# Kernel tuning notes

Measured on AMD Instinct MI355X. Metric: run time of the kernel, lower is better.

Reference implementation:

```python
import jax, jax.numpy as jnp
import numpy as np
from jax import lax

NQ = 4      # num_qubits
DEPTH = 2
DIM = 2 ** NQ  # 16

def _maxpool2(x):
    # MaxPool2d(kernel_size=2, stride=1), NCHW
    return lax.reduce_window(x, -jnp.inf, lax.max, (1, 1, 2, 2), (1, 1, 1, 1), 'VALID')

def _conv(x, w, b, stride, pad):
    y = lax.conv_general_dilated(x, w, (stride, stride), [(pad, pad), (pad, pad)],
                                 dimension_numbers=('NCHW', 'OIHW', 'NCHW'))
    return y + b[None, :, None, None]

def _apply_1q(state, gate, q):
    # state: (B, 16) complex64; gate: (2,2) shared or (B,2,2) per-sample. wire 0 = MSB.
    B = state.shape[0]
    s = state.reshape(B, 2 ** q, 2, 2 ** (NQ - 1 - q))
    sub = 'ij,bljr->blir' if gate.ndim == 2 else 'bij,bljr->blir'
    return jnp.einsum(sub, gate, s).reshape(B, DIM)

def _quantum_head(angles, weights):
    # Batched statevector simulation of: RX(angles[i]) encoding, then DEPTH x
    # [RY(w) on every wire, CZ chain], then <Z_0>, <Z_1>.
    B = angles.shape[0]
    state = jnp.zeros((B, DIM), jnp.complex64).at[:, 0].set(1.0)
    for q in range(NQ):  # RX encoding (per-sample angles)
        t = angles[:, q] * 0.5
        c = jnp.cos(t).astype(jnp.complex64)
        s = (-1j) * jnp.sin(t).astype(jnp.complex64)
        gate = jnp.stack([jnp.stack([c, s], -1), jnp.stack([s, c], -1)], -2)  # (B,2,2)
        state = _apply_1q(state, gate, q)
    idxs = jnp.arange(DIM)
    w_idx = 0
    for _ in range(DEPTH):
        for q in range(NQ):  # RY(weights) shared across batch
            t = weights[w_idx] * 0.5
            w_idx += 1
            c, s = jnp.cos(t), jnp.sin(t)
            gate = jnp.stack([jnp.stack([c, -s]), jnp.stack([s, c])]).astype(jnp.complex64)
            state = _apply_1q(state, gate, q)
        for q in range(NQ - 1):  # CZ(q, q+1): -1 phase where both bits set
            both = ((idxs >> (NQ - 1 - q)) & 1) & ((idxs >> (NQ - 2 - q)) & 1)
            phase = jnp.where(both == 1, -1.0, 1.0).astype(jnp.complex64)
            state = state * phase[None, :]
    probs = state.real ** 2 + state.imag ** 2  # (B,16) float32
    logits = []
    for q in range(2):  # expval PauliZ on wires 0,1
        sign = 1.0 - 2.0 * ((idxs >> (NQ - 1 - q)) & 1).astype(jnp.float32)
        logits.append(probs @ sign)
    return jnp.stack(logits, -1)  # (B,2)


def setup_inputs() -> dict:
    key = jax.random.key(0)
    ks = jax.random.split(key, 12)
    x = jax.random.normal(ks[0], (256, 3, 250, 250), jnp.float32)
    w1 = jax.random.normal(ks[1], (6, 3, 5, 5), jnp.float32) * 0.05
    b1 = jnp.zeros((6,), jnp.float32)
    w2 = jax.random.normal(ks[2], (15, 6, 3, 3), jnp.float32) * 0.05
    b2 = jnp.zeros((15,), jnp.float32)
    fc1_w = jax.random.normal(ks[3], (120, 55815), jnp.float32) * 0.004
    fc1_b = jnp.zeros((120,), jnp.float32)
    fc2_w = jax.random.normal(ks[4], (84, 120), jnp.float32) * 0.09
    fc2_b = jnp.zeros((84,), jnp.float32)
    fc3_w = jax.random.normal(ks[5], (4, 84), jnp.float32) * 0.1
    fc3_b = jnp.zeros((4,), jnp.float32)
    qweights = jax.random.normal(ks[6], (NQ * DEPTH,), jnp.float32)
    return {'x': x, 'w1': w1, 'b1': b1, 'w2': w2, 'b2': b2,
            'fc1_w': fc1_w, 'fc1_b': fc1_b, 'fc2_w': fc2_w, 'fc2_b': fc2_b,
            'fc3_w': fc3_w, 'fc3_b': fc3_b, 'qweights': qweights}


def reference(x, w1, b1, w2, b2, fc1_w, fc1_b, fc2_w, fc2_b, fc3_w, fc3_b, qweights):
    # Dropout layers act as identity (eval mode).
    h = jax.nn.relu(_conv(x, w1, b1, stride=2, pad=1))   # (B,6,124,124)
    h = _maxpool2(h)                                      # (B,6,123,123)
    h = jax.nn.relu(_conv(h, w2, b2, stride=2, pad=1))   # (B,15,62,62)
    h = _maxpool2(h)                                      # (B,15,61,61)
    h = h.reshape(h.shape[0], -1)                         # (B,55815)
    h = jax.nn.relu(h @ fc1_w.T + fc1_b)
    h = jax.nn.relu(h @ fc2_w.T + fc2_b)
    angles = h @ fc3_w.T + fc3_b                          # (B,4)
    logits = _quantum_head(angles, qweights)              # (B,2)
    return jax.nn.softmax(logits, axis=-1)
```

## Files before the change

kernel.cpp:

```cpp
#include <hip/hip_runtime.h>
#include <hip/hip_bf16.h>
#include <math.h>

#define B 256
#define FC1_K   55815
#define FC1_N   120
#define FC2_N   84
#define KP        57344
#define FC1_SPLIT 256
#define FC1_KC    (KP / FC1_SPLIT)

typedef __attribute__((ext_vector_type(8))) short bf16x8;
typedef __attribute__((ext_vector_type(4))) float f32x4;

static __device__ __forceinline__ unsigned short bf16_bits(float f) {
    __hip_bfloat16 h = __float2bfloat16(f);
    return *(unsigned short*)&h;
}

#define ASYNC_CP(g, l) __builtin_amdgcn_global_load_lds( \
    (const __attribute__((address_space(1))) void*)(g),  \
    (__attribute__((address_space(3))) void*)(l), 4, 0, 0)

__global__ __launch_bounds__(256) void prep_kernel(
    const float* __restrict__ w1, const float* __restrict__ w2,
    const float* __restrict__ fc1_w,
    float* __restrict__ w1p, float* __restrict__ w2p,
    float* __restrict__ zeros, unsigned short* __restrict__ wb) {
    const int n = blockIdx.y;
    const int k0 = blockIdx.x * 2048 + threadIdx.x * 8;
    bf16x8 v8;
    #pragma unroll
    for (int i = 0; i < 8; ++i) v8[i] = 0;
    if (n < FC1_N) {
        const float* src = fc1_w + (size_t)n * FC1_K + k0;
        if (k0 + 8 <= FC1_K) {
            #pragma unroll
            for (int i = 0; i < 8; ++i) v8[i] = (short)bf16_bits(src[i]);
        } else {
            #pragma unroll
            for (int i = 0; i < 8; ++i)
                if (k0 + i < FC1_K) v8[i] = (short)bf16_bits(src[i]);
        }
    }
    *(bf16x8*)(wb + (size_t)n * KP + k0) = v8;

    if (blockIdx.x == 0 && n == 0) {
        int t = threadIdx.x;
        for (int f = t; f < 450; f += 256) {
            int o = f % 6, tap = f / 6;
            int kx = tap % 5, r2 = tap / 5, ky = r2 % 5, c = r2 / 5;
            w1p[f] = w1[(o * 3 + c) * 25 + ky * 5 + kx];
        }
        for (int f = t; f < 810; f += 256) {
            int o = f % 15, tap = f / 15;
            int kx = tap % 3, r2 = tap / 3, ky = r2 % 3, c = r2 / 3;
            w2p[f] = w2[(o * 6 + c) * 9 + ky * 3 + kx];
        }
        if (t < 64) zeros[t] = 0.f;
    }
}

__global__ __launch_bounds__(256) void conv1_pool1_kernel(
    const float* __restrict__ x, const float* __restrict__ w1p,
    const float* __restrict__ b1, unsigned short* __restrict__ pool1,
    const float* __restrict__ zeros) {
    __shared__ __align__(16) float in_t[19 * 256 + 8];
    __shared__ __align__(16) unsigned short out_t[6 * 8 * 132];

    const int tid = threadIdx.x;
    const int wave = tid >> 6, lane = tid & 63;
    const int PB = 7 * blockIdx.x;
    const int b  = blockIdx.y;
    const int cg = tid & 31, rr = tid >> 5;
    const int iyb = 2 * PB - 1;

    float acc[4][6];
    #pragma unroll
    for (int j = 0; j < 4; ++j)
        #pragma unroll
        for (int o = 0; o < 6; ++o) acc[j][o] = b1[o];

    for (int c = 0; c < 3; ++c) {
        __syncthreads();
        const float* xp = x + (size_t)(b * 3 + c) * 62500;
        #pragma unroll
        for (int i = 0; i < 19; ++i) {
            int chunk = wave * 19 + i;
            int f = chunk * 64 + lane;
            int row = f >> 8, m = f & 255;
            int iy = iyb + row, col = m - 1;
            const float* g = ((unsigned)iy < 250u && (unsigned)col < 250u)
                             ? (xp + iy * 250 + col) : zeros;
            ASYNC_CP(g, &in_t[chunk * 64]);
        }
        __syncthreads();
        const float* wc = w1p + c * 150;
        #pragma unroll
        for (int ky = 0; ky < 5; ++ky) {
            const float* rp = &in_t[(2 * rr + ky) * 256 + 8 * cg];
            float f[12];
            float4 v0 = *(const float4*)rp;
            float4 v1 = *(const float4*)(rp + 4);
            float4 v2 = *(const float4*)(rp + 8);
            f[0]=v0.x; f[1]=v0.y; f[2]=v0.z; f[3]=v0.w;
            f[4]=v1.x; f[5]=v1.y; f[6]=v1.z; f[7]=v1.w;
            f[8]=v2.x; f[9]=v2.y; f[10]=v2.z; f[11]=v2.w;
            #pragma unroll
            for (int kx = 0; kx < 5; ++kx) {
                const float* wp = wc + (ky * 5 + kx) * 6;
                #pragma unroll
                for (int j = 0; j < 4; ++j) {
                    float xv = f[2 * j + kx];
                    #pragma unroll
                    for (int o = 0; o < 6; ++o) acc[j][o] += xv * wp[o];
                }
            }
        }
    }
    #pragma unroll
    for (int o = 0; o < 6; ++o) {
        unsigned short h0 = bf16_bits(fmaxf(acc[0][o], 0.f));
        unsigned short h1 = bf16_bits(fmaxf(acc[1][o], 0.f));
        unsigned short h2 = bf16_bits(fmaxf(acc[2][o], 0.f));
        unsigned short h3 = bf16_bits(fmaxf(acc[3][o], 0.f));
        uint2 pk;
        pk.x = (unsigned)h0 | ((unsigned)h1 << 16);
        pk.y = (unsigned)h2 | ((unsigned)h3 << 16);
        *(uint2*)&out_t[(o * 8 + rr) * 132 + 4 * cg] = pk;
    }
    __syncthreads();
    for (int it = tid; it < 6 * 7 * 32; it += 256) {
        int g = it & 31, rem = it >> 5;
        int pyl = rem % 7, oc = rem / 7;
        int py = PB + pyl;
        if (py >= 123) continue;
        const unsigned short* q0 = &out_t[(oc * 8 + pyl) * 132 + 4 * g];
        const unsigned short* q1 = q0 + 132;
        uint2 ua = *(const uint2*)q0;
        uint2 ub = *(const uint2*)q1;
        unsigned short va[5] = {(unsigned short)(ua.x & 0xffff), (unsigned short)(ua.x >> 16),
                                (unsigned short)(ua.y & 0xffff), (unsigned short)(ua.y >> 16), q0[4]};
        unsigned short vb[5] = {(unsigned short)(ub.x & 0xffff), (unsigned short)(ub.x >> 16),
                                (unsigned short)(ub.y & 0xffff), (unsigned short)(ub.y >> 16), q1[4]};
        unsigned short* dst = pool1 + ((size_t)(b * 6 + oc) * 123 + py) * 128;
        #pragma unroll
        for (int j = 0; j < 4; ++j) {
            int px = 4 * g + j;
            if (px >= 127) continue;
            unsigned short m = 0;
            if (px <= 122) {
                unsigned short m0 = va[j] > va[j+1] ? va[j] : va[j+1];
                unsigned short m1 = vb[j] > vb[j+1] ? vb[j] : vb[j+1];
                m = m0 > m1 ? m0 : m1;
            }
            dst[1 + px] = m;
        }
        if (g == 0) dst[0] = 0;
    }
}

__global__ __launch_bounds__(128) void conv2_pool2_kernel(
    const unsigned short* __restrict__ pool1, const float* __restrict__ w2p,
    const float* __restrict__ b2, unsigned short* __restrict__ A,
    const unsigned int* __restrict__ zerosu) {
    __shared__ __align__(16) unsigned int in2[17 * 64 + 4];
    __shared__ __align__(16) unsigned short out2[15 * 8 * 68];

    const int tid = threadIdx.x;
    const int wave = tid >> 6, lane = tid & 63;
    const int PB = 7 * blockIdx.x;
    const int b  = blockIdx.y;
    const int cg = tid & 15, rr = tid >> 4;
    const int iyb = 2 * PB - 1;

    float acc[4][15];
    #pragma unroll
    for (int j = 0; j < 4; ++j)
        #pragma unroll
        for (int o = 0; o < 15; ++o) acc[j][o] = b2[o];

    const unsigned int* p1u = (const unsigned int*)pool1;
    for (int c = 0; c < 6; ++c) {
        __syncthreads();
        const unsigned int* pp = p1u + (size_t)(b * 6 + c) * (123 * 64);
        #pragma unroll
        for (int i = 0; i < 9; ++i) {
            int chunk = wave * 9 + i;
            if (chunk < 17) {
                int f = chunk * 64 + lane;
                int row = f >> 6, off = f & 63;
                int iy = iyb + row;
                const unsigned int* g = ((unsigned)iy < 123u)
                                        ? (pp + iy * 64 + off) : zerosu;
                ASYNC_CP(g, &in2[chunk * 64]);
            }
        }
        __syncthreads();
        #pragma unroll
        for (int ky = 0; ky < 3; ++ky) {
            const unsigned int* rp = &in2[(2 * rr + ky) * 64 + 4 * cg];
            uint4 u4 = *(const uint4*)rp;
            unsigned int u5 = rp[4];
            float f[10];
            f[0] = __uint_as_float(u4.x << 16); f[1] = __uint_as_float(u4.x & 0xffff0000u);
            f[2] = __uint_as_float(u4.y << 16); f[3] = __uint_as_float(u4.y & 0xffff0000u);
            f[4] = __uint_as_float(u4.z << 16); f[5] = __uint_as_float(u4.z & 0xffff0000u);
            f[6] = __uint_as_float(u4.w << 16); f[7] = __uint_as_float(u4.w & 0xffff0000u);
            f[8] = __uint_as_float(u5  << 16);  f[9] = __uint_as_float(u5  & 0xffff0000u);
            #pragma unroll
            for (int kx = 0; kx < 3; ++kx) {
                const float* wp = w2p + (c * 9 + ky * 3 + kx) * 15;
                #pragma unroll
                for (int j = 0; j < 4; ++j) {
                    float xv = f[2 * j + kx];
                    #pragma unroll
                    for (int o = 0; o < 15; ++o) acc[j][o] += xv * wp[o];
                }
            }
        }
    }
    #pragma unroll
    for (int o = 0; o < 15; ++o) {
        unsigned short h0 = bf16_bits(fmaxf(acc[0][o], 0.f));
        unsigned short h1 = bf16_bits(fmaxf(acc[1][o], 0.f));
        unsigned short h2 = bf16_bits(fmaxf(acc[2][o], 0.f));
        unsigned short h3 = bf16_bits(fmaxf(acc[3][o], 0.f));
        uint2 pk;
        pk.x = (unsigned)h0 | ((unsigned)h1 << 16);
        pk.y = (unsigned)h2 | ((unsigned)h3 << 16);
        *(uint2*)&out2[(o * 8 + rr) * 68 + 4 * cg] = pk;
    }
    __syncthreads();
    for (int it = tid; it < 15 * 7 * 16; it += 128) {
        int g = it & 15, rem = it >> 4;
        int pyl = rem % 7, oc = rem / 7;
        int py = PB + pyl;
        if (py >= 61) continue;
        const unsigned short* q0 = &out2[(oc * 8 + pyl) * 68 + 4 * g];
        const unsigned short* q1 = q0 + 68;
        uint2 ua = *(const uint2*)q0;
        uint2 ub = *(const uint2*)q1;
        unsigned short va[5] = {(unsigned short)(ua.x & 0xffff), (unsigned short)(ua.x >> 16),
                                (unsigned short)(ua.y & 0xffff), (unsigned short)(ua.y >> 16), q0[4]};
        unsigned short vb[5] = {(unsigned short)(ub.x & 0xffff), (unsigned short)(ub.x >> 16),
                                (unsigned short)(ub.y & 0xffff), (unsigned short)(ub.y >> 16), q1[4]};
        #pragma unroll
        for (int j = 0; j < 4; ++j) {
            int px = 4 * g + j;
            if (px < 61) {
                unsigned short m0 = va[j] > va[j+1] ? va[j] : va[j+1];
                unsigned short m1 = vb[j] > vb[j+1] ? vb[j] : vb[j+1];
                unsigned short m = m0 > m1 ? m0 : m1;
                A[(size_t)b * KP + (oc * 61 + py) * 61 + px] = m;
            }
        }
    }
}

__global__ __launch_bounds__(256) void fc1_mfma_kernel(
    const __hip_bfloat16* __restrict__ A, const __hip_bfloat16* __restrict__ W,
    float* __restrict__ partial) {
    const int wave = threadIdx.x >> 6, lane = threadIdx.x & 63;
    const int mrow = lane & 15, quad = lane >> 4;
    const int m0 = blockIdx.x * 128 + wave * 32;
    const int k0 = blockIdx.y * FC1_KC;

    f32x4 acc[2][8];
    #pragma unroll
    for (int i = 0; i < 2; ++i)
        #pragma unroll
        for (int j = 0; j < 8; ++j) acc[i][j] = (f32x4){0.f, 0.f, 0.f, 0.f};

    const short* Ap = (const short*)A;
    const short* Wp = (const short*)W;
    for (int ks = 0; ks < FC1_KC; ks += 32) {
        const int kk = k0 + ks + quad * 8;
        const bf16x8 a0 = *(const bf16x8*)(Ap + (size_t)(m0 + mrow) * KP + kk);
        const bf16x8 a1 = *(const bf16x8*)(Ap + (size_t)(m0 + 16 + mrow) * KP + kk);
        #pragma unroll
        for (int nt = 0; nt < 8; ++nt) {
            const bf16x8 bb = *(const bf16x8*)(Wp + (size_t)(nt * 16 + mrow) * KP + kk);
            acc[0][nt] = __builtin_amdgcn_mfma_f32_16x16x32_bf16(a0, bb, acc[0][nt], 0, 0, 0);
            acc[1][nt] = __builtin_amdgcn_mfma_f32_16x16x32_bf16(a1, bb, acc[1][nt], 0, 0, 0);
        }
    }
    float* po = partial + (size_t)blockIdx.y * (256 * 128);
    #pragma unroll
    for (int mt = 0; mt < 2; ++mt)
        #pragma unroll
        for (int nt = 0; nt < 8; ++nt)
            #pragma unroll
            for (int r = 0; r < 4; ++r)
                po[(m0 + mt * 16 + quad * 4 + r) * 128 + nt * 16 + mrow] = acc[mt][nt][r];
}

__global__ __launch_bounds__(512) void tail_kernel(
    const float* __restrict__ partial, const float* __restrict__ fc1_b,
    const float* __restrict__ fc2_w, const float* __restrict__ fc2_b,
    const float* __restrict__ fc3_w, const float* __restrict__ fc3_b,
    const float* __restrict__ qw, float* __restrict__ out) {
    __shared__ float h1p[4][FC1_N];
    __shared__ float h1[FC1_N];
    __shared__ float h2[FC2_N];
    __shared__ float ang[4];
    int b = blockIdx.x;
    int t = threadIdx.x;
    int grp = t >> 7, tt = t & 127;

    if (tt < FC1_N) {
        const float* p = partial + b * 128 + tt;
        float sum = 0.f;
        #pragma unroll 8
        for (int s = grp * 64; s < grp * 64 + 64; ++s) sum += p[(size_t)s * (256 * 128)];
        h1p[grp][tt] = sum;
    }
    __syncthreads();
    if (t < FC1_N)
        h1[t] = fmaxf(h1p[0][t] + h1p[1][t] + h1p[2][t] + h1p[3][t] + fc1_b[t], 0.f);
    __syncthreads();
    if (t < FC2_N) {
        float acc = fc2_b[t];
        const float* w = fc2_w + t * FC1_N;
        for (int k = 0; k < FC1_N; ++k) acc += h1[k] * w[k];
        h2[t] = fmaxf(acc, 0.f);
    }
    __syncthreads();
    if (t < 4) {
        float acc = fc3_b[t];
        const float* w = fc3_w + t * FC2_N;
        for (int k = 0; k < FC2_N; ++k) acc += h2[k] * w[k];
        ang[t] = acc;
    }
    __syncthreads();
    if (t < 16) {
        const int lane = t;
        float sr = (lane == 0) ? 1.f : 0.f, si = 0.f;
        #pragma unroll
        for (int q = 0; q < 4; ++q) {
            float th = ang[q] * 0.5f;
            float c = __cosf(th), s = __sinf(th);
            int mask = 8 >> q;
            float pr = __shfl_xor(sr, mask, 16);
            float pi = __shfl_xor(si, mask, 16);
            float nr = c * sr + s * pi;
            float ni = c * si - s * pr;
            sr = nr; si = ni;
        }
        int widx = 0;
        #pragma unroll
        for (int d = 0; d < 2; ++d) {
            #pragma unroll
            for (int q = 0; q < 4; ++q) {
                float th = qw[widx++] * 0.5f;
                float c = __cosf(th), s = __sinf(th);
                int mask = 8 >> q;
                float pr = __shfl_xor(sr, mask, 16);
                float pi = __shfl_xor(si, mask, 16);
                float sg = (lane & mask) ? s : -s;
                sr = c * sr + sg * pr;
                si = c * si + sg * pi;
            }
            #pragma unroll
            for (int q = 0; q < 3; ++q) {
                int m1 = 8 >> q, m2 = 4 >> q;
                if ((lane & m1) && (lane & m2)) { sr = -sr; si = -si; }
            }
        }
        float p = sr * sr + si * si;
        float v0 = (lane & 8) ? -p : p;
        float v1 = (lane & 4) ? -p : p;
        #pragma unroll
        for (int off = 8; off >= 1; off >>= 1) {
            v0 += __shfl_xor(v0, off, 16);
            v1 += __shfl_xor(v1, off, 16);
        }
        if (lane == 0) {
            float m = fmaxf(v0, v1);
            float e0 = expf(v0 - m), e1 = expf(v1 - m);
            float inv = 1.f / (e0 + e1);
            out[b * 2 + 0] = e0 * inv;
            out[b * 2 + 1] = e1 * inv;
        }
    }
}

extern "C" void kernel_launch(void* const* d_in, const int* in_sizes, int n_in,
                              void* d_out, int out_size, void* d_ws, size_t ws_size,
                              hipStream_t stream) {
    const float* x     = (const float*)d_in[0];
    const float* w1    = (const float*)d_in[1];
    const float* b1    = (const float*)d_in[2];
    const float* w2    = (const float*)d_in[3];
    const float* b2    = (const float*)d_in[4];
    const float* fc1_w = (const float*)d_in[5];
    const float* fc1_b = (const float*)d_in[6];
    const float* fc2_w = (const float*)d_in[7];
    const float* fc2_b = (const float*)d_in[8];
    const float* fc3_w = (const float*)d_in[9];
    const float* fc3_b = (const float*)d_in[10];
    const float* qw    = (const float*)d_in[11];
    float* out = (float*)d_out;

    char* ws = (char*)d_ws;
    const size_t O_POOL1  = 0;
    const size_t O_A      = O_POOL1 + 48365568;
    const size_t O_W      = O_A + 29360128;
    const size_t O_PART   = O_W + 14680064;
    const size_t O_W1P    = O_PART + 33554432;
    const size_t O_W2P    = O_W1P + 2048;
    const size_t O_ZERO   = O_W2P + 4096;
    unsigned short* pool1   = (unsigned short*)(ws + O_POOL1);
    __hip_bfloat16* A_bf16  = (__hip_bfloat16*)(ws + O_A);
    __hip_bfloat16* W_bf16  = (__hip_bfloat16*)(ws + O_W);
    float*          partial = (float*)(ws + O_PART);
    float*          w1p     = (float*)(ws + O_W1P);
    float*          w2p     = (float*)(ws + O_W2P);
    float*          zeros   = (float*)(ws + O_ZERO);

    prep_kernel<<<dim3(KP / 2048, 128), 256, 0, stream>>>(
        w1, w2, fc1_w, w1p, w2p, zeros, (unsigned short*)W_bf16);
    conv1_pool1_kernel<<<dim3(18, B), 256, 0, stream>>>(x, w1p, b1, pool1, zeros);
    conv2_pool2_kernel<<<dim3(9, B), 128, 0, stream>>>(pool1, w2p, b2,
                                                       (unsigned short*)A_bf16,
                                                       (const unsigned int*)zeros);
    fc1_mfma_kernel<<<dim3(2, FC1_SPLIT), 256, 0, stream>>>(A_bf16, W_bf16, partial);
    tail_kernel<<<B, 512, 0, stream>>>(partial, fc1_b, fc2_w, fc2_b,
                                       fc3_w, fc3_b, qw, out);
}
```

Measured before the change: 421.4 us.

## Fold weight prep into conv1 and use fp16 dot2 in conv2

Removes the separate prep kernel. Its fc1 weight bf16 conversion now runs as extra blocks of the conv1 launch, and the conv weights are read or repacked directly inside each conv kernel. The pool1 intermediate changes from bf16 to fp16 so that conv2 can use packed fdot2 instructions with fp32 accumulation, with the fp16 weights staged in LDS. This halves conv2's multiply-add instruction count and drops a kernel launch, at the cost of fp16 range and precision for the activations. The zero buffer is now written by conv1 blocks while other conv1 blocks may already be reading it, which is a race.

Result: slower. 448.9 us (+6.5%).

```diff
diff --git a/kernel.cpp b/kernel.cpp
--- a/kernel.cpp
+++ b/kernel.cpp
@@ -1,5 +1,6 @@
 #include <hip/hip_runtime.h>
 #include <hip/hip_bf16.h>
+#include <hip/hip_fp16.h>
 #include <math.h>
 
 #define B 256
@@ -12,59 +13,51 @@
 
 typedef __attribute__((ext_vector_type(8))) short bf16x8;
 typedef __attribute__((ext_vector_type(4))) float f32x4;
+typedef _Float16 half2_t __attribute__((ext_vector_type(2)));
 
 static __device__ __forceinline__ unsigned short bf16_bits(float f) {
     __hip_bfloat16 h = __float2bfloat16(f);
     return *(unsigned short*)&h;
 }
+static __device__ __forceinline__ unsigned short f16_bits(float f) {
+    __half h = __float2half(f);
+    return *(unsigned short*)&h;
+}
+static __device__ __forceinline__ half2_t h2_from_u32(unsigned int u) {
+    return __builtin_bit_cast(half2_t, u);
+}
 
 #define ASYNC_CP(g, l) __builtin_amdgcn_global_load_lds( \
     (const __attribute__((address_space(1))) void*)(g),  \
     (__attribute__((address_space(3))) void*)(l), 4, 0, 0)
 
-__global__ __launch_bounds__(256) void prep_kernel(
-    const float* __restrict__ w1, const float* __restrict__ w2,
-    const float* __restrict__ fc1_w,
-    float* __restrict__ w1p, float* __restrict__ w2p,
-    float* __restrict__ zeros, unsigned short* __restrict__ wb) {
-    const int n = blockIdx.y;
-    const int k0 = blockIdx.x * 2048 + threadIdx.x * 8;
-    bf16x8 v8;
-    #pragma unroll
-    for (int i = 0; i < 8; ++i) v8[i] = 0;
-    if (n < FC1_N) {
-        const float* src = fc1_w + (size_t)n * FC1_K + k0;
-        if (k0 + 8 <= FC1_K) {
-            #pragma unroll
-            for (int i = 0; i < 8; ++i) v8[i] = (short)bf16_bits(src[i]);
-        } else {
-            #pragma unroll
-            for (int i = 0; i < 8; ++i)
-                if (k0 + i < FC1_K) v8[i] = (short)bf16_bits(src[i]);
-        }
-    }
-    *(bf16x8*)(wb + (size_t)n * KP + k0) = v8;
-
-    if (blockIdx.x == 0 && n == 0) {
-        int t = threadIdx.x;
-        for (int f = t; f < 450; f += 256) {
-            int o = f % 6, tap = f / 6;
-            int kx = tap % 5, r2 = tap / 5, ky = r2 % 5, c = r2 / 5;
-            w1p[f] = w1[(o * 3 + c) * 25 + ky * 5 + kx];
-        }
-        for (int f = t; f < 810; f += 256) {
-            int o = f % 15, tap = f / 15;
-            int kx = tap % 3, r2 = tap / 3, ky = r2 % 3, c = r2 / 3;
-            w2p[f] = w2[(o * 6 + c) * 9 + ky * 3 + kx];
-        }
-        if (t < 64) zeros[t] = 0.f;
-    }
-}
-
-__global__ __launch_bounds__(256) void conv1_pool1_kernel(
-    const float* __restrict__ x, const float* __restrict__ w1p,
-    const float* __restrict__ b1, unsigned short* __restrict__ pool1,
-    const float* __restrict__ zeros) {
+__global__ __launch_bounds__(256) void conv1_fused_kernel(
+    const float* __restrict__ x, const float* __restrict__ w1,
+    const float* __restrict__ b1, const float* __restrict__ fc1_w,
+    unsigned short* __restrict__ pool1, float* __restrict__ zeros,
+    unsigned short* __restrict__ wb) {
+    if (blockIdx.x >= 18) {
+        int wid = (blockIdx.x - 18) * 256 + blockIdx.y;
+        int kb = wid >> 7, n = wid & 127;
+        int k0 = kb * 2048 + threadIdx.x * 8;
+        bf16x8 v8;
+        #pragma unroll
+        for (int i = 0; i < 8; ++i) v8[i] = 0;
+        if (n < FC1_N) {
+            const float* src = fc1_w + (size_t)n * FC1_K + k0;
+            if (k0 + 8 <= FC1_K) {
+                #pragma unroll
+                for (int i = 0; i < 8; ++i) v8[i] = (short)bf16_bits(src[i]);
+            } else {
+                #pragma unroll
+                for (int i = 0; i < 8; ++i)
+                    if (k0 + i < FC1_K) v8[i] = (short)bf16_bits(src[i]);
+            }
+        }
+        *(bf16x8*)(wb + (size_t)n * KP + k0) = v8;
+        return;
+    }
+
     __shared__ __align__(16) float in_t[19 * 256 + 8];
     __shared__ __align__(16) unsigned short out_t[6 * 8 * 132];
 
@@ -74,6 +67,8 @@
     const int b  = blockIdx.y;
     const int cg = tid & 31, rr = tid >> 5;
     const int iyb = 2 * PB - 1;
+
+    if (tid < 64) zeros[tid] = 0.f;
 
     float acc[4][6];
     #pragma unroll
@@ -95,7 +90,6 @@
             ASYNC_CP(g, &in_t[chunk * 64]);
         }
         __syncthreads();
-        const float* wc = w1p + c * 150;
         #pragma unroll
         for (int ky = 0; ky < 5; ++ky) {
             const float* rp = &in_t[(2 * rr + ky) * 256 + 8 * cg];
@@ -108,22 +102,22 @@
             f[8]=v2.x; f[9]=v2.y; f[10]=v2.z; f[11]=v2.w;
             #pragma unroll
             for (int kx = 0; kx < 5; ++kx) {
-                const float* wp = wc + (ky * 5 + kx) * 6;
                 #pragma unroll
                 for (int j = 0; j < 4; ++j) {
                     float xv = f[2 * j + kx];
                     #pragma unroll
-                    for (int o = 0; o < 6; ++o) acc[j][o] += xv * wp[o];
+                    for (int o = 0; o < 6; ++o)
+                        acc[j][o] += xv * w1[(o * 3 + c) * 25 + ky * 5 + kx];
                 }
             }
         }
     }
     #pragma unroll
     for (int o = 0; o < 6; ++o) {
-        unsigned short h0 = bf16_bits(fmaxf(acc[0][o], 0.f));
-        unsigned short h1 = bf16_bits(fmaxf(acc[1][o], 0.f));
-        unsigned short h2 = bf16_bits(fmaxf(acc[2][o], 0.f));
-        unsigned short h3 = bf16_bits(fmaxf(acc[3][o], 0.f));
+        unsigned short h0 = f16_bits(fmaxf(acc[0][o], 0.f));
+        unsigned short h1 = f16_bits(fmaxf(acc[1][o], 0.f));
+        unsigned short h2 = f16_bits(fmaxf(acc[2][o], 0.f));
+        unsigned short h3 = f16_bits(fmaxf(acc[3][o], 0.f));
         uint2 pk;
         pk.x = (unsigned)h0 | ((unsigned)h1 << 16);
         pk.y = (unsigned)h2 | ((unsigned)h3 << 16);
@@ -161,10 +155,10 @@
 }
 
 __global__ __launch_bounds__(128) void conv2_pool2_kernel(
-    const unsigned short* __restrict__ pool1, const float* __restrict__ w2p,
-    const float* __restrict__ b2, unsigned short* __restrict__ A,
-    const unsigned int* __restrict__ zerosu) {
-    __shared__ __align__(16) unsigned int in2[17 * 64 + 4];
+    const unsigned short* __restrict__ pool1, const float* __restrict__ w2,
+    const float* __restrict__ b2, unsigned short* __restrict__ A) {
+    __shared__ __align__(16) unsigned int in2[17 * 64 + 8];
+    __shared__ __align__(16) unsigned int wlds[540];
     __shared__ __align__(16) unsigned short out2[15 * 8 * 68];
 
     const int tid = threadIdx.x;
@@ -174,6 +168,17 @@
     const int cg = tid & 15, rr = tid >> 4;
     const int iyb = 2 * PB - 1;
 
+    for (int f = tid; f < 540; f += 128) {
+        int pr = f & 1, g = f >> 1;
+        int o = g % 15, r = g / 15, ky = r % 3, c = r / 3;
+        const float* wsrc = w2 + (o * 6 + c) * 9 + ky * 3;
+        unsigned int pk;
+        if (pr == 0) pk = (unsigned)f16_bits(wsrc[0]) | ((unsigned)f16_bits(wsrc[1]) << 16);
+        else         pk = (unsigned)f16_bits(wsrc[2]);
+        wlds[((c * 3 + ky) * 15 + o) * 2 + pr] = pk;
+    }
+    if (tid < 8) in2[17 * 64 + tid] = 0;
+
     float acc[4][15];
     #pragma unroll
     for (int j = 0; j < 4; ++j)
@@ -188,34 +193,38 @@
         for (int i = 0; i < 9; ++i) {
             int chunk = wave * 9 + i;
             if (chunk < 17) {
-                int f = chunk * 64 + lane;
-                int row = f >> 6, off = f & 63;
-                int iy = iyb + row;
-                const unsigned int* g = ((unsigned)iy < 123u)
-                                        ? (pp + iy * 64 + off) : zerosu;
-                ASYNC_CP(g, &in2[chunk * 64]);
+                int iy = iyb + chunk;
+                if ((unsigned)iy < 123u) {
+                    ASYNC_CP(pp + iy * 64 + lane, &in2[chunk * 64]);
+                } else {
+                    in2[chunk * 64 + lane] = 0;
+                }
             }
         }
         __syncthreads();
         #pragma unroll
         for (int ky = 0; ky < 3; ++ky) {
             const unsigned int* rp = &in2[(2 * rr + ky) * 64 + 4 * cg];
-            uint4 u4 = *(const uint4*)rp;
-            unsigned int u5 = rp[4];
-            float f[10];
-            f[0] = __uint_as_float(u4.x << 16); f[1] = __uint_as_float(u4.x & 0xffff0000u);
-            f[2] = __uint_as_float(u4.y << 16); f[3] = __uint_as_float(u4.y & 0xffff0000u);
-            f[4] = __uint_as_float(u4.z << 16); f[5] = __uint_as_float(u4.z & 0xffff0000u);
-            f[6] = __uint_as_float(u4.w << 16); f[7] = __uint_as_float(u4.w & 0xffff0000u);
-            f[8] = __uint_as_float(u5  << 16);  f[9] = __uint_as_float(u5  & 0xffff0000u);
-            #pragma unroll
-            for (int kx = 0; kx < 3; ++kx) {
-                const float* wp = w2p + (c * 9 + ky * 3 + kx) * 15;
+            half2_t dd[5];
+            {
+                uint4 u4 = *(const uint4*)rp;
+                unsigned int u5 = rp[4];
+                dd[0] = h2_from_u32(u4.x); dd[1] = h2_from_u32(u4.y);
+                dd[2] = h2_from_u32(u4.z); dd[3] = h2_from_u32(u4.w);
+                dd[4] = h2_from_u32(u5);
+            }
+            const unsigned int* wrow = &wlds[(c * 3 + ky) * 30];
+            unsigned int wv[30];
+            #pragma unroll
+            for (int i = 0; i < 30; ++i) wv[i] = wrow[i];
+            #pragma unroll
+            for (int j = 0; j < 4; ++j) {
                 #pragma unroll
-                for (int j = 0; j < 4; ++j) {
-                    float xv = f[2 * j + kx];
-                    #pragma unroll
-                    for (int o = 0; o < 15; ++o) acc[j][o] += xv * wp[o];
+                for (int o = 0; o < 15; ++o) {
+                    acc[j][o] = __builtin_amdgcn_fdot2(dd[j],     h2_from_u32(wv[o * 2]),
+                                                       acc[j][o], false);
+                    acc[j][o] = __builtin_amdgcn_fdot2(dd[j + 1], h2_from_u32(wv[o * 2 + 1]),
+                                                       acc[j][o], false);
                 }
             }
         }
@@ -407,23 +416,17 @@
     const size_t O_A      = O_POOL1 + 48365568;
     const size_t O_W      = O_A + 29360128;
     const size_t O_PART   = O_W + 14680064;
-    const size_t O_W1P    = O_PART + 33554432;
-    const size_t O_W2P    = O_W1P + 2048;
-    const size_t O_ZERO   = O_W2P + 4096;
+    const size_t O_ZERO   = O_PART + 33554432;
     unsigned short* pool1   = (unsigned short*)(ws + O_POOL1);
     __hip_bfloat16* A_bf16  = (__hip_bfloat16*)(ws + O_A);
     __hip_bfloat16* W_bf16  = (__hip_bfloat16*)(ws + O_W);
     float*          partial = (float*)(ws + O_PART);
-    float*          w1p     = (float*)(ws + O_W1P);
-    float*          w2p     = (float*)(ws + O_W2P);
     float*          zeros   = (float*)(ws + O_ZERO);
 
-    prep_kernel<<<dim3(KP / 2048, 128), 256, 0, stream>>>(
-        w1, w2, fc1_w, w1p, w2p, zeros, (unsigned short*)W_bf16);
-    conv1_pool1_kernel<<<dim3(18, B), 256, 0, stream>>>(x, w1p, b1, pool1, zeros);
-    conv2_pool2_kernel<<<dim3(9, B), 128, 0, stream>>>(pool1, w2p, b2,
-                                                       (unsigned short*)A_bf16,
-                                                       (const unsigned int*)zeros);
+    conv1_fused_kernel<<<dim3(32, B), 256, 0, stream>>>(
+        x, w1, b1, fc1_w, pool1, zeros, (unsigned short*)W_bf16);
+    conv2_pool2_kernel<<<dim3(9, B), 128, 0, stream>>>(pool1, w2, b2,
+                                                       (unsigned short*)A_bf16);
     fc1_mfma_kernel<<<dim3(2, FC1_SPLIT), 256, 0, stream>>>(A_bf16, W_bf16, partial);
     tail_kernel<<<B, 512, 0, stream>>>(partial, fc1_b, fc2_w, fc2_b,
                                        fc3_w, fc3_b, qw, out);
```
